# Kernel tuning notes

Measured on AMD Instinct MI355X. Metric: run time of the kernel, lower is better.

## Reference

```python
import jax, jax.numpy as jnp
import numpy as np

INPUT_DIM = 1024
HIDDEN_DIM = 1024
BATCH = 8
SEQ = 2048


def setup_inputs() -> dict:
    key = jax.random.key(0)
    ks = jax.random.split(key, 7)
    s = 1.0 / np.sqrt(INPUT_DIM)
    return {
        "subgraph_embeddings": jax.random.normal(ks[0], (BATCH, SEQ, INPUT_DIM), dtype=jnp.float32),
        "Wq": jax.random.uniform(ks[1], (INPUT_DIM, HIDDEN_DIM), jnp.float32, -s, s),
        "bq": jax.random.uniform(ks[2], (HIDDEN_DIM,), jnp.float32, -s, s),
        "Wk": jax.random.uniform(ks[3], (INPUT_DIM, HIDDEN_DIM), jnp.float32, -s, s),
        "bk": jax.random.uniform(ks[4], (HIDDEN_DIM,), jnp.float32, -s, s),
        "Wv": jax.random.uniform(ks[5], (INPUT_DIM, HIDDEN_DIM), jnp.float32, -s, s),
        "bv": jax.random.uniform(ks[6], (HIDDEN_DIM,), jnp.float32, -s, s),
    }


def reference(subgraph_embeddings, Wq, bq, Wk, bk, Wv, bv):
    x = subgraph_embeddings  # [B, S, D]
    Q = jnp.einsum('bsd,dh->bsh', x, Wq) + bq
    K = jnp.einsum('bsd,dh->bsh', x, Wk) + bk
    V = jnp.einsum('bsd,dh->bsh', x, Wv) + bv
    scale = jnp.sqrt(jnp.float32(HIDDEN_DIM))
    scores = jnp.einsum('bqh,bkh->bqk', Q, K) / scale  # [B, S, S]
    weights = jax.nn.softmax(scores, axis=-1)
    return jnp.einsum('bqk,bkh->bqh', weights, V)
```

## Files before the change

### kernel.cpp

```cpp
#include <hip/hip_runtime.h>
#include <hip/hip_bf16.h>
#include <stdint.h>

typedef unsigned short u16;
typedef unsigned int u32;
typedef __attribute__((ext_vector_type(8))) short bf16x8;
typedef __attribute__((ext_vector_type(4))) float f32x4;

#define S_LEN 2048
#define D_DIM 1024
#define H_DIM 1024
#define BATCH 8
#define M_TOTAL (BATCH * S_LEN)

__device__ __forceinline__ u16 f2b(float f) {
  u32 u = __builtin_bit_cast(u32, f);
  u32 r = (u + 0x7fffu + ((u >> 16) & 1u)) >> 16;
  return (u16)r;
}

__global__ __launch_bounds__(256) void cast_x_kernel(const float* __restrict__ in,
                                                     u16* __restrict__ out, int n8) {
  int i = blockIdx.x * 256 + threadIdx.x;
  if (i >= n8) return;
  const float4* p = (const float4*)in;
  float4 a = p[2 * i], b = p[2 * i + 1];
  u32 w0 = (u32)f2b(a.x) | ((u32)f2b(a.y) << 16);
  u32 w1 = (u32)f2b(a.z) | ((u32)f2b(a.w) << 16);
  u32 w2 = (u32)f2b(b.x) | ((u32)f2b(b.y) << 16);
  u32 w3 = (u32)f2b(b.z) | ((u32)f2b(b.w) << 16);
  ((uint4*)out)[i] = make_uint4(w0, w1, w2, w3);
}

__global__ __launch_bounds__(256) void wcast_all_kernel(
    const float* __restrict__ Wq, const float* __restrict__ Wk,
    const float* __restrict__ Wv, const float* __restrict__ bq,
    const float* __restrict__ bk, u16* __restrict__ Wtqk,
    u16* __restrict__ Wtv, float* __restrict__ bqk, float* __restrict__ lsum) {
  __shared__ float tile[32][33];
  int z = blockIdx.z;
  const float* W = (z == 0) ? Wq : (z == 1) ? Wk : Wv;
  u16* Wt = (z == 0) ? Wtqk : (z == 1) ? (Wtqk + 1024 * 1024) : Wtv;
  int h0 = blockIdx.x * 32, d0 = blockIdx.y * 32;
  int tx = threadIdx.x & 31, ty = threadIdx.x >> 5;
#pragma unroll
  for (int r = ty; r < 32; r += 8)
    tile[r][tx] = W[(size_t)(d0 + r) * H_DIM + h0 + tx];
  if (blockIdx.x == 0 && blockIdx.y == 0) {
    if (z == 0) {
      for (int i = threadIdx.x; i < 1024; i += 256) bqk[i] = bq[i];
    } else if (z == 1) {
      for (int i = threadIdx.x; i < 1024; i += 256) bqk[1024 + i] = bk[i];
    } else {
      for (int i = threadIdx.x; i < M_TOTAL; i += 256) lsum[i] = 0.f;
    }
  }
  __syncthreads();
#pragma unroll
  for (int r = ty; r < 32; r += 8)
    Wt[(size_t)(h0 + r) * D_DIM + d0 + tx] = f2b(tile[tx][r]);
}

template <int BIAS, int EPI, bool OUT_BF16>
__global__ __launch_bounds__(512, 2) void gemm256(
    const u16* __restrict__ A, const u16* __restrict__ Bt, void* __restrict__ Cout,
    const float* __restrict__ bias, float* __restrict__ lsum,
    int M, int N, int K, int lda, int ldb, int ldc,
    long long aBatch, long long bBatch, long long cBatch, float scale) {
  __shared__ __align__(16) u16 As[2][256 * 64];
  __shared__ __align__(16) u16 Bs[2][256 * 64];
  const int tid = threadIdx.x;
  const int wave = tid >> 6, lane = tid & 63;
  const int quad = lane >> 4, lr = lane & 15;
  const int wm = (wave >> 2) * 128, wn = (wave & 3) * 64;
  const int row0 = blockIdx.x * 256, col0 = blockIdx.y * 256;
  A += (size_t)blockIdx.z * (size_t)aBatch;
  Bt += (size_t)blockIdx.z * (size_t)bBatch;

  f32x4 acc[8][4] = {};

  auto AsL = (__attribute__((address_space(3))) char*)&As[0][0];
  auto BsL = (__attribute__((address_space(3))) char*)&Bs[0][0];
  const char* Ab = (const char*)A;
  const char* Bb = (const char*)Bt;

  auto stage_a = [&](int buf, int h, int k0) {
#pragma unroll
    for (int rr = 0; rr < 2; ++rr) {
      int chunk = rr * 512 + tid;
      int row = chunk >> 3;
      int cs = (chunk & 7) ^ (row & 7);
      const void* g = Ab + (((size_t)(row0 + h * 128 + row) * lda +
                             (size_t)(k0 + cs * 8)) * 2);
      __builtin_amdgcn_global_load_lds(
          (const __attribute__((address_space(1))) void*)g,
          (__attribute__((address_space(3))) void*)(AsL + (size_t)buf * 32768 +
                                                   (size_t)(h * 1024 + chunk) * 16),
          16, 0, 0);
    }
  };
  auto stage_b = [&](int buf, int h, int k0) {
#pragma unroll
    for (int rr = 0; rr < 2; ++rr) {
      int chunk = rr * 512 + tid;
      int row = chunk >> 3;
      int cs = (chunk & 7) ^ (row & 7);
      const void* g = Bb + (((size_t)(col0 + h * 128 + row) * ldb +
                             (size_t)(k0 + cs * 8)) * 2);
      __builtin_amdgcn_global_load_lds(
          (const __attribute__((address_space(1))) void*)g,
          (__attribute__((address_space(3))) void*)(BsL + (size_t)buf * 32768 +
                                                   (size_t)(h * 1024 + chunk) * 16),
          16, 0, 0);
    }
  };

#define READ_A(MH)                                                              \
  _Pragma("unroll") for (int ksi = 0; ksi < 2; ++ksi)                           \
  _Pragma("unroll") for (int i = 0; i < 4; ++i) {                               \
    int r = wm + ((MH) * 4 + i) * 16 + lr;                                      \
    int cc = (ksi * 4 + quad) ^ (r & 7);                                        \
    afr[ksi][i] = *(const bf16x8*)&As[cur][r * 64 + cc * 8];                    \
  }
#define READ_B(NH)                                                              \
  _Pragma("unroll") for (int ksi = 0; ksi < 2; ++ksi)                           \
  _Pragma("unroll") for (int j = 0; j < 2; ++j) {                               \
    int r = wn + ((NH) * 2 + j) * 16 + lr;                                      \
    int cc = (ksi * 4 + quad) ^ (r & 7);                                        \
    bfr[NH][j][ksi] = *(const bf16x8*)&Bs[cur][r * 64 + cc * 8];                \
  }
#define MFMA_QUAD(MH, NH)                                                       \
  _Pragma("unroll") for (int ksi = 0; ksi < 2; ++ksi)                           \
  _Pragma("unroll") for (int i = 0; i < 4; ++i)                                 \
  _Pragma("unroll") for (int j = 0; j < 2; ++j)                                 \
    acc[(MH) * 4 + i][(NH) * 2 + j] = __builtin_amdgcn_mfma_f32_16x16x32_bf16(  \
        afr[ksi][i], bfr[NH][j][ksi], acc[(MH) * 4 + i][(NH) * 2 + j], 0, 0, 0);

#define WAIT_LGKM()                                        \
  asm volatile("s_waitcnt lgkmcnt(0)" ::: "memory");       \
  __builtin_amdgcn_sched_barrier(0)

  const int nkt = K >> 6;

  stage_a(0, 0, 0);
  stage_b(0, 0, 0);
  stage_b(0, 1, 0);
  stage_a(0, 1, 0);
  asm volatile("s_waitcnt vmcnt(0)" ::: "memory");
  __builtin_amdgcn_sched_barrier(0);
  __builtin_amdgcn_s_barrier();

  bf16x8 afr[2][4];
  bf16x8 bfr[2][2][2];

  for (int t = 0; t < nkt - 1; ++t) {
    const int cur = t & 1, nxt = cur ^ 1;
    const int kn = (t + 1) << 6;
    READ_A(0);
    READ_B(0);
    stage_a(nxt, 0, kn);
    stage_b(nxt, 0, kn);
    WAIT_LGKM();
    __builtin_amdgcn_s_setprio(1);
    MFMA_QUAD(0, 0);
    __builtin_amdgcn_s_setprio(0);
    READ_B(1);
    stage_b(nxt, 1, kn);
    stage_a(nxt, 1, kn);
    WAIT_LGKM();
    __builtin_amdgcn_s_setprio(1);
    MFMA_QUAD(0, 1);
    __builtin_amdgcn_s_setprio(0);
    READ_A(1);
    WAIT_LGKM();
    __builtin_amdgcn_s_setprio(1);
    MFMA_QUAD(1, 0);
    __builtin_amdgcn_s_setprio(0);
    __builtin_amdgcn_s_setprio(1);
    MFMA_QUAD(1, 1);
    __builtin_amdgcn_s_setprio(0);
    asm volatile("s_waitcnt vmcnt(0)" ::: "memory");
    __builtin_amdgcn_sched_barrier(0);
    __builtin_amdgcn_s_barrier();
  }
  {
    const int cur = (nkt - 1) & 1;
    READ_A(0);
    READ_B(0);
    READ_B(1);
    WAIT_LGKM();
    MFMA_QUAD(0, 0);
    MFMA_QUAD(0, 1);
    READ_A(1);
    WAIT_LGKM();
    MFMA_QUAD(1, 0);
    MFMA_QUAD(1, 1);
  }
#undef READ_A
#undef READ_B
#undef MFMA_QUAD
#undef WAIT_LGKM

  const long long lrow0 = (long long)blockIdx.z * M + row0;

  if constexpr (EPI == 1) {
    u16* C = (u16*)Cout + (size_t)blockIdx.z * (size_t)cBatch;
#pragma unroll
    for (int i = 0; i < 8; ++i) {
#pragma unroll
      for (int ii = 0; ii < 4; ++ii) {
        int r = wm + i * 16 + quad * 4 + ii;
        float rowsum = 0.f;
#pragma unroll
        for (int j = 0; j < 4; ++j) {
          float e = __expf(acc[i][j][ii] * scale);
          rowsum += e;
          C[(size_t)(row0 + r) * ldc + (col0 + wn + j * 16 + lr)] = f2b(e);
        }
#pragma unroll
        for (int off = 1; off < 16; off <<= 1) rowsum += __shfl_xor(rowsum, off);
        if (lr == 0) atomicAdd(lsum + lrow0 + r, rowsum);
      }
    }
    return;
  }

#pragma unroll
  for (int i = 0; i < 8; ++i) {
#pragma unroll
    for (int ii = 0; ii < 4; ++ii) {
      int r = wm + i * 16 + quad * 4 + ii;
      float radd = 0.f, rmul = 1.f;
      if (BIAS == 2) radd = bias[row0 + r];
      if (EPI == 2) rmul = 1.0f / lsum[lrow0 + r];
#pragma unroll
      for (int j = 0; j < 4; ++j) {
        int c = col0 + wn + j * 16 + lr;
        float v = acc[i][j][ii] * rmul + radd;
        if (BIAS == 1) v += bias[c];
        if constexpr (OUT_BF16) {
          u16* C = (u16*)Cout + (size_t)blockIdx.z * (size_t)cBatch;
          C[(size_t)(row0 + r) * ldc + c] = f2b(v);
        } else {
          float* C = (float*)Cout + (size_t)blockIdx.z * (size_t)cBatch;
          C[(size_t)(row0 + r) * ldc + c] = v;
        }
      }
    }
  }
}

extern "C" void kernel_launch(void* const* d_in, const int* in_sizes, int n_in,
                              void* d_out, int out_size, void* d_ws, size_t ws_size,
                              hipStream_t stream) {
  const float* x = (const float*)d_in[0];
  const float* Wq = (const float*)d_in[1];
  const float* bq = (const float*)d_in[2];
  const float* Wk = (const float*)d_in[3];
  const float* bk = (const float*)d_in[4];
  const float* Wv = (const float*)d_in[5];
  const float* bv = (const float*)d_in[6];
  float* out = (float*)d_out;

  char* ws = (char*)d_ws;
  u16* xb = (u16*)ws;   ws += (size_t)M_TOTAL * D_DIM * 2;
  u16* Wtqk = (u16*)ws; ws += (size_t)2 * H_DIM * D_DIM * 2;
  u16* Wtv = (u16*)ws;  ws += (size_t)H_DIM * D_DIM * 2;
  u16* QKm = (u16*)ws;  ws += (size_t)M_TOTAL * 2 * H_DIM * 2;
  u16* Vt = (u16*)ws;   ws += (size_t)BATCH * H_DIM * S_LEN * 2;
  u16* Sm = (u16*)ws;   ws += (size_t)BATCH * S_LEN * S_LEN * 2;
  float* bqk = (float*)ws;  ws += 2048 * 4;
  float* lsum = (float*)ws; ws += (size_t)M_TOTAL * 4;

  cast_x_kernel<<<(M_TOTAL * D_DIM / 8 + 255) / 256, 256, 0, stream>>>(
      x, xb, M_TOTAL * D_DIM / 8);
  wcast_all_kernel<<<dim3(32, 32, 3), 256, 0, stream>>>(
      Wq, Wk, Wv, bq, bk, Wtqk, Wtv, bqk, lsum);

  gemm256<1, 0, true><<<dim3(64, 8, 1), 512, 0, stream>>>(
      xb, Wtqk, QKm, bqk, nullptr, M_TOTAL, 2 * H_DIM, D_DIM,
      D_DIM, D_DIM, 2 * H_DIM, 0, 0, 0, 0.f);

  gemm256<2, 0, true><<<dim3(4, 8, BATCH), 512, 0, stream>>>(
      Wtv, xb, Vt, bv, nullptr, H_DIM, S_LEN, D_DIM,
      D_DIM, D_DIM, S_LEN,
      0LL, (long long)S_LEN * D_DIM, (long long)H_DIM * S_LEN, 0.f);

  gemm256<0, 1, true><<<dim3(8, 8, BATCH), 512, 0, stream>>>(
      QKm, QKm + H_DIM, Sm, nullptr, lsum, S_LEN, S_LEN, H_DIM,
      2 * H_DIM, 2 * H_DIM, S_LEN,
      (long long)S_LEN * 2 * H_DIM, (long long)S_LEN * 2 * H_DIM,
      (long long)S_LEN * S_LEN, 0.03125f);

  gemm256<0, 2, false><<<dim3(8, 4, BATCH), 512, 0, stream>>>(
      Sm, Vt, out, nullptr, lsum, S_LEN, H_DIM, S_LEN,
      S_LEN, S_LEN, H_DIM,
      (long long)S_LEN * S_LEN, (long long)H_DIM * S_LEN,
      (long long)S_LEN * H_DIM, 0.f);
}
```

Before: 378.5 us.

## Deepen GEMM LDS pipeline to prefetch two k-tiles ahead with quarter staging

Restructures the GEMM main loop so global-to-LDS loads are issued two k-tiles ahead instead of one, waiting with a partial vmcnt so one tile's loads stay in flight across iterations. The staging is split by row-quarters that match what each MFMA phase has finished reading, so the current buffer is refilled piecewise, separated by workgroup barriers. Explicit lgkmcnt waits are removed and the compiler is left to order LDS reads. The aim is to hide global load latency behind more MFMA work, at the cost of extra barriers per iteration and tight correctness dependencies on the buffer reuse ordering.

```diff
diff --git a/kernel.cpp b/kernel.cpp
--- a/kernel.cpp
+++ b/kernel.cpp
@@ -84,33 +84,33 @@
   const char* Ab = (const char*)A;
   const char* Bb = (const char*)Bt;
 
-  auto stage_a = [&](int buf, int h, int k0) {
+  auto stage_aq = [&](int buf, int q, int k0) {
 #pragma unroll
     for (int rr = 0; rr < 2; ++rr) {
-      int chunk = rr * 512 + tid;
-      int row = chunk >> 3;
-      int cs = (chunk & 7) ^ (row & 7);
-      const void* g = Ab + (((size_t)(row0 + h * 128 + row) * lda +
-                             (size_t)(k0 + cs * 8)) * 2);
+      int idx = rr * 512 + tid;
+      int i = idx >> 3, ch = idx & 7;
+      int row = ((i >> 6) << 7) | (q << 6) | (i & 63);
+      int cs = ch ^ (row & 7);
+      const void* g = Ab + (((size_t)(row0 + row) * lda + (size_t)(k0 + cs * 8)) * 2);
       __builtin_amdgcn_global_load_lds(
           (const __attribute__((address_space(1))) void*)g,
           (__attribute__((address_space(3))) void*)(AsL + (size_t)buf * 32768 +
-                                                   (size_t)(h * 1024 + chunk) * 16),
+                                                   (size_t)(row * 8 + ch) * 16),
           16, 0, 0);
     }
   };
-  auto stage_b = [&](int buf, int h, int k0) {
+  auto stage_bq = [&](int buf, int q, int k0) {
 #pragma unroll
     for (int rr = 0; rr < 2; ++rr) {
-      int chunk = rr * 512 + tid;
-      int row = chunk >> 3;
-      int cs = (chunk & 7) ^ (row & 7);
-      const void* g = Bb + (((size_t)(col0 + h * 128 + row) * ldb +
-                             (size_t)(k0 + cs * 8)) * 2);
+      int idx = rr * 512 + tid;
+      int i = idx >> 3, ch = idx & 7;
+      int row = ((i >> 5) << 6) | (q << 5) | (i & 31);
+      int cs = ch ^ (row & 7);
+      const void* g = Bb + (((size_t)(col0 + row) * ldb + (size_t)(k0 + cs * 8)) * 2);
       __builtin_amdgcn_global_load_lds(
           (const __attribute__((address_space(1))) void*)g,
           (__attribute__((address_space(3))) void*)(BsL + (size_t)buf * 32768 +
-                                                   (size_t)(h * 1024 + chunk) * 16),
+                                                   (size_t)(row * 8 + ch) * 16),
           16, 0, 0);
     }
   };
@@ -136,70 +136,80 @@
     acc[(MH) * 4 + i][(NH) * 2 + j] = __builtin_amdgcn_mfma_f32_16x16x32_bf16(  \
         afr[ksi][i], bfr[NH][j][ksi], acc[(MH) * 4 + i][(NH) * 2 + j], 0, 0, 0);
 
-#define WAIT_LGKM()                                        \
-  asm volatile("s_waitcnt lgkmcnt(0)" ::: "memory");       \
+#define BAR()                                              \
+  __builtin_amdgcn_s_barrier();                            \
   __builtin_amdgcn_sched_barrier(0)
 
   const int nkt = K >> 6;
 
-  stage_a(0, 0, 0);
-  stage_b(0, 0, 0);
-  stage_b(0, 1, 0);
-  stage_a(0, 1, 0);
-  asm volatile("s_waitcnt vmcnt(0)" ::: "memory");
+  stage_aq(0, 0, 0); stage_bq(0, 0, 0); stage_bq(0, 1, 0); stage_aq(0, 1, 0);
+  stage_aq(1, 0, 64); stage_bq(1, 0, 64); stage_bq(1, 1, 64); stage_aq(1, 1, 64);
+  asm volatile("s_waitcnt vmcnt(8)" ::: "memory");
   __builtin_amdgcn_sched_barrier(0);
-  __builtin_amdgcn_s_barrier();
+  BAR();
 
   bf16x8 afr[2][4];
   bf16x8 bfr[2][2][2];
 
-  for (int t = 0; t < nkt - 1; ++t) {
-    const int cur = t & 1, nxt = cur ^ 1;
-    const int kn = (t + 1) << 6;
+  for (int t = 0; t <= nkt - 3; ++t) {
+    const int cur = t & 1;
+    const int kn = (t + 2) << 6;
     READ_A(0);
     READ_B(0);
-    stage_a(nxt, 0, kn);
-    stage_b(nxt, 0, kn);
-    WAIT_LGKM();
     __builtin_amdgcn_s_setprio(1);
     MFMA_QUAD(0, 0);
     __builtin_amdgcn_s_setprio(0);
+    BAR();
     READ_B(1);
-    stage_b(nxt, 1, kn);
-    stage_a(nxt, 1, kn);
-    WAIT_LGKM();
+    stage_aq(cur, 0, kn);
+    stage_bq(cur, 0, kn);
     __builtin_amdgcn_s_setprio(1);
     MFMA_QUAD(0, 1);
     __builtin_amdgcn_s_setprio(0);
+    BAR();
     READ_A(1);
-    WAIT_LGKM();
+    stage_bq(cur, 1, kn);
     __builtin_amdgcn_s_setprio(1);
     MFMA_QUAD(1, 0);
     __builtin_amdgcn_s_setprio(0);
+    BAR();
+    stage_aq(cur, 1, kn);
     __builtin_amdgcn_s_setprio(1);
     MFMA_QUAD(1, 1);
     __builtin_amdgcn_s_setprio(0);
+    asm volatile("s_waitcnt vmcnt(8)" ::: "memory");
+    __builtin_amdgcn_sched_barrier(0);
+    BAR();
+  }
+  {
+    const int cur = (nkt - 2) & 1;
+    READ_A(0);
+    READ_B(0);
+    MFMA_QUAD(0, 0);
+    READ_B(1);
+    MFMA_QUAD(0, 1);
+    READ_A(1);
+    MFMA_QUAD(1, 0);
+    MFMA_QUAD(1, 1);
     asm volatile("s_waitcnt vmcnt(0)" ::: "memory");
     __builtin_amdgcn_sched_barrier(0);
-    __builtin_amdgcn_s_barrier();
+    BAR();
   }
   {
     const int cur = (nkt - 1) & 1;
     READ_A(0);
     READ_B(0);
+    MFMA_QUAD(0, 0);
     READ_B(1);
-    WAIT_LGKM();
-    MFMA_QUAD(0, 0);
     MFMA_QUAD(0, 1);
     READ_A(1);
-    WAIT_LGKM();
     MFMA_QUAD(1, 0);
     MFMA_QUAD(1, 1);
   }
 #undef READ_A
 #undef READ_B
 #undef MFMA_QUAD
-#undef WAIT_LGKM
+#undef BAR
 
   const long long lrow0 = (long long)blockIdx.z * M + row0;
 
```

Result: slower. 401.3 us (+6.0%).
